# Kernel optimization log

Measured on AMD Instinct MI355X. Metric: run time of the kernel, lower is better.

The kernel has to match this reference:

```python
import jax, jax.numpy as jnp
import numpy as np

EPS = 1e-15
ATANH_CLIP = 1.0 - 1e-5
C = 1.0  # ball.c = |k|, k = -1.0
SQC = 1.0  # sqrt(C)


def _artanh(x):
    return jnp.arctanh(jnp.clip(x, -ATANH_CLIP, ATANH_CLIP))


def _norm(x):
    return jnp.linalg.norm(x, axis=-1, keepdims=True)


def mobius_add(x, y):
    x2 = jnp.sum(x * x, axis=-1, keepdims=True)
    y2 = jnp.sum(y * y, axis=-1, keepdims=True)
    xy = jnp.sum(x * y, axis=-1, keepdims=True)
    num = (1.0 + 2.0 * C * xy + C * y2) * x + (1.0 - C * x2) * y
    den = 1.0 + 2.0 * C * xy + (C ** 2) * x2 * y2
    return num / jnp.maximum(den, EPS)


def mobius_matvec(M, x):
    # x: [..., d_in], M: [d_out, d_in]
    x_norm = jnp.maximum(_norm(x), EPS)
    mx = x @ M.T
    mx_norm_raw = _norm(mx)
    mx_norm = jnp.maximum(mx_norm_raw, EPS)
    res = jnp.tanh(mx_norm / x_norm * _artanh(SQC * x_norm)) * mx / (mx_norm * SQC)
    return jnp.where(mx_norm_raw <= EPS, 0.0, res)


def mobius_pointwise_mul(w, x):
    x_norm = jnp.maximum(_norm(x), EPS)
    wx = w * x
    wx_norm_raw = _norm(wx)
    wx_norm = jnp.maximum(wx_norm_raw, EPS)
    res = jnp.tanh(wx_norm / x_norm * _artanh(SQC * x_norm)) * wx / (wx_norm * SQC)
    return jnp.where(wx_norm_raw <= EPS, 0.0, res)


def expmap0(u):
    un = jnp.maximum(_norm(u), EPS)
    return jnp.tanh(SQC * un) * u / (SQC * un)


def logmap0(y):
    yn = jnp.maximum(_norm(y), EPS)
    return _artanh(SQC * yn) * y / (SQC * yn)


def one_rnn_transform(W, h, U, x, b):
    Wh = mobius_matvec(W, h)
    Ux = mobius_matvec(U, x)
    return mobius_add(mobius_add(Wh, Ux), b)


def gru_cell(x, hx, weight_ih, weight_hh, bias):
    W_ir, W_ih, W_iz = jnp.split(weight_ih, 3, axis=0)
    W_hr, W_hh, W_hz = jnp.split(weight_hh, 3, axis=0)
    b_r, b_h, b_z = bias[0], bias[1], bias[2]
    z_t = jax.nn.sigmoid(logmap0(one_rnn_transform(W_hz, hx, W_iz, x, b_z)))
    r_t = jax.nn.sigmoid(logmap0(one_rnn_transform(W_hr, hx, W_ir, x, b_r)))
    rh_t = mobius_pointwise_mul(r_t, hx)
    h_tilde = one_rnn_transform(W_hh, rh_t, W_ih, x, b_h)
    delta_h = mobius_add(-hx, h_tilde)
    return mobius_add(hx, mobius_pointwise_mul(z_t, delta_h))


def gru_layer(x_seq, h0, weight_ih, weight_hh, bias):
    def step(hx, xt):
        h = gru_cell(xt, hx, weight_ih, weight_hh, bias)
        return h, h
    h_last, outs = jax.lax.scan(step, h0, x_seq)
    return outs, h_last


def setup_inputs() -> dict:
    key = jax.random.key(0)
    ks = jax.random.split(key, 8)
    T, B, D, H = 256, 64, 512, 512
    stdv = 1.0 / np.sqrt(H)
    inp = {
        # hyperbolic_input=True -> points must lie inside the unit ball; scale small
        "input": jax.random.normal(ks[0], (T, B, D), jnp.float32) * 0.01,
        "h0": jnp.zeros((2, B, H), jnp.float32),
        "weight_ih_1": jax.random.uniform(ks[1], (3 * H, D), jnp.float32, -stdv, stdv),
        "weight_ih_2": jax.random.uniform(ks[2], (3 * H, H), jnp.float32, -stdv, stdv),
        "weight_hh_1": jax.random.uniform(ks[3], (3 * H, H), jnp.float32, -stdv, stdv),
        "weight_hh_2": jax.random.uniform(ks[4], (3 * H, H), jnp.float32, -stdv, stdv),
        # biases initialized as expmap0(randn * 1e-5)
        "bias_1": expmap0(jax.random.normal(ks[5], (3, H), jnp.float32) * 1e-5),
        "bias_2": expmap0(jax.random.normal(ks[6], (3, H), jnp.float32) * 1e-5),
    }
    return inp


def reference(input, h0, weight_ih_1, weight_ih_2, weight_hh_1, weight_hh_2, bias_1, bias_2):
    # hyperbolic_input=True and hyperbolic_hidden_state0=True -> no initial expmap0
    out1, h_last1 = gru_layer(input, h0[0], weight_ih_1, weight_hh_1, bias_1)
    out2, h_last2 = gru_layer(out1, h0[1], weight_ih_2, weight_hh_2, bias_2)
    ht = jnp.stack([h_last1, h_last2])
    return out2, ht
```

## Files before the change

kernel.cpp:

```cpp
#include <hip/hip_runtime.h>
#include <hip/hip_fp16.h>
#include <math.h>
#include <stdint.h>


#define T_  256
#define B_  64
#define H_  512
#define G3_ 1536
#define EPSF 1e-15f
#define CLIPF (1.0f - 1e-5f)
#define SCOPE_AGENT __HIP_MEMORY_SCOPE_AGENT

typedef _Float16 v2h __attribute__((ext_vector_type(2)));

__device__ __forceinline__ float fdot2_(unsigned int w, unsigned int h, float c){
#if __has_builtin(__builtin_amdgcn_fdot2)
  return __builtin_amdgcn_fdot2(__builtin_bit_cast(v2h, w), __builtin_bit_cast(v2h, h), c, false);
#else
  const __half2 wh = __builtin_bit_cast(__half2, w);
  const __half2 hh = __builtin_bit_cast(__half2, h);
  return c + __low2float(wh)*__low2float(hh) + __high2float(wh)*__high2float(hh);
#endif
}

__device__ __forceinline__ float artanh_c(float x){
  x = fminf(fmaxf(x, -CLIPF), CLIPF);
  return 0.5f * logf((1.0f + x) / (1.0f - x));
}
__device__ __forceinline__ float sigmoidf_(float x){ return 1.0f/(1.0f+expf(-x)); }
__device__ __forceinline__ float hsum4(float4 v){ return (v.x+v.y)+(v.z+v.w); }

__device__ __forceinline__ void postf(unsigned long long* p, float x, unsigned tag){
  unsigned long long v = ((unsigned long long)tag << 32) |
                         (unsigned long long)__float_as_uint(x);
  __hip_atomic_store(p, v, __ATOMIC_RELAXED, SCOPE_AGENT);
}
__device__ __forceinline__ float pollf(const unsigned long long* p, unsigned tag){
  unsigned long long v = __hip_atomic_load(p, __ATOMIC_RELAXED, SCOPE_AGENT);
  while ((unsigned)(v >> 32) != tag)
    v = __hip_atomic_load(p, __ATOMIC_RELAXED, SCOPE_AGENT);
  return __uint_as_float((unsigned)v);
}

template<int NS>
__device__ __forceinline__ void wave_reduce_store(float (&v)[NS], float* red, int tid){
  #pragma unroll
  for (int off = 32; off > 0; off >>= 1)
    #pragma unroll
    for (int s = 0; s < NS; s++) v[s] += __shfl_xor(v[s], off);
  if ((tid & 63) == 0)
    #pragma unroll
    for (int s = 0; s < NS; s++) red[s*8 + (tid >> 6)] = v[s];
}

__global__ void k_prep_ih(const float* __restrict__ Wih, float* __restrict__ WihT){
  int i = blockIdx.x * blockDim.x + threadIdx.x;
  if (i >= H_ * G3_) return;
  int k = i / G3_, n = i % G3_;
  WihT[i] = Wih[n * H_ + k];
}

__device__ __forceinline__ uint4 pack8h(const float* s){
  __half2 p0 = __halves2half2(__float2half_rn(s[0]), __float2half_rn(s[1]));
  __half2 p1 = __halves2half2(__float2half_rn(s[2]), __float2half_rn(s[3]));
  __half2 p2 = __halves2half2(__float2half_rn(s[4]), __float2half_rn(s[5]));
  __half2 p3 = __halves2half2(__float2half_rn(s[6]), __float2half_rn(s[7]));
  uint4 r;
  r.x = __builtin_bit_cast(unsigned int, p0);
  r.y = __builtin_bit_cast(unsigned int, p1);
  r.z = __builtin_bit_cast(unsigned int, p2);
  r.w = __builtin_bit_cast(unsigned int, p3);
  return r;
}

__global__ void k_prep_hhR(const float* __restrict__ Whh, uint4* __restrict__ WzrR,
                           uint4* __restrict__ WhcR){
  int i = blockIdx.x * blockDim.x + threadIdx.x;
  if (i < 65536){
    int w = i >> 14, rem = i & 16383;
    int ii = rem >> 9, tid = rem & 511;
    int c = tid & 255, ks = tid >> 8;
    int j = 128*w + (c & 127);
    int row = (c < 128) ? (1024 + j) : j;
    int k0 = ks*256 + ii*8;
    WzrR[i] = pack8h(Whh + row*H_ + k0);
  } else {
    int e = i - 65536;
    int w = e >> 13, rem = e & 8191;
    int q = rem >> 11, rem2 = rem & 2047;
    int ii = rem2 >> 7, c = rem2 & 127;
    int row = 512 + 128*w + c;
    int k0 = q*128 + ii*8;
    WhcR[e] = pack8h(Whh + row*H_ + k0);
  }
}

__global__ __launch_bounds__(256) void k_gemm(const float* __restrict__ A,
                                              const float* __restrict__ Bt,
                                              float* __restrict__ C){
  const int N = G3_, K = H_;
  const int mbase = blockIdx.x * 64, nbase = blockIdx.y * 64;
  __shared__ float As[32][65];
  __shared__ float Bs[32][65];
  const int tid = threadIdx.x;
  const int tm = tid >> 4, tn = tid & 15;
  float acc[4][4] = {};
  for (int k0 = 0; k0 < K; k0 += 32){
    #pragma unroll
    for (int i = 0; i < 8; i++){
      int e = tid + 256*i;
      int m = e >> 5, k = e & 31;
      As[k][m] = A[(size_t)(mbase + m) * K + k0 + k];
      int kk = e >> 6, n = e & 63;
      Bs[kk][n] = Bt[(size_t)(k0 + kk) * N + nbase + n];
    }
    __syncthreads();
    #pragma unroll
    for (int kk = 0; kk < 32; kk++){
      float av[4], bv[4];
      #pragma unroll
      for (int i = 0; i < 4; i++) av[i] = As[kk][tm*4+i];
      #pragma unroll
      for (int j = 0; j < 4; j++) bv[j] = Bs[kk][tn*4+j];
      #pragma unroll
      for (int i = 0; i < 4; i++)
        #pragma unroll
        for (int j = 0; j < 4; j++)
          acc[i][j] = fmaf(av[i], bv[j], acc[i][j]);
    }
    __syncthreads();
  }
  #pragma unroll
  for (int i = 0; i < 4; i++)
    #pragma unroll
    for (int j = 0; j < 4; j++)
      C[(size_t)(mbase + tm*4 + i) * N + nbase + tn*4 + j] = acc[i][j];
}

__global__ void k_nonlin(const float* __restrict__ X, float* __restrict__ D){
  const int row = blockIdx.x;
  const int lane = threadIdx.x;
  const float* x = X + (size_t)row * H_;
  float s = 0.0f;
  for (int k = lane; k < H_; k += 64){ float v = x[k]; s = fmaf(v, v, s); }
  #pragma unroll
  for (int off = 32; off > 0; off >>= 1) s += __shfl_xor(s, off);
  const float xn = fmaxf(sqrtf(s), EPSF);
  const float art = artanh_c(xn);
  float* drow = D + (size_t)row * G3_;
  for (int g = 0; g < 3; g++){
    float* mx = drow + g * H_;
    float s2 = 0.0f;
    for (int k = lane; k < H_; k += 64){ float v = mx[k]; s2 = fmaf(v, v, s2); }
    #pragma unroll
    for (int off = 32; off > 0; off >>= 1) s2 += __shfl_xor(s2, off);
    const float raw = sqrtf(s2);
    const float mn = fmaxf(raw, EPSF);
    const float scale = (raw <= EPSF) ? 0.0f : (tanhf(mn / xn * art) / mn);
    for (int k = lane; k < H_; k += 64) mx[k] *= scale;
  }
}

__global__ __launch_bounds__(512, 1) void k_scan(
    const float* __restrict__ D,
    const uint4* __restrict__ WzrR,
    const uint4* __restrict__ WhcR,
    const float* __restrict__ bias,
    const float* __restrict__ h0,
    float* __restrict__ outbuf,
    float* __restrict__ hlast,
    unsigned long long* __restrict__ hS,
    unsigned long long* __restrict__ wvS,
    unsigned long long* __restrict__ S1s,
    unsigned long long* __restrict__ S3s,
    unsigned long long* __restrict__ S4s)
{
  const int blk = blockIdx.x;
  const int b = blk & 63, w = blk >> 6;
  const int tid = threadIdx.x;
  const int lane = tid & 63, wave = tid >> 6;
  __shared__ __align__(16) __half hh[H_];
  __shared__ __align__(16) float hf[H_];
  __shared__ __align__(16) __half wvh[H_];
  __shared__ __align__(16) float ph[512];
  __shared__ __align__(16) float red[96];
  __shared__ __align__(16) float redW[8];
  __shared__ __align__(16) float xr[16];

  unsigned long long* hRow  = hS  + b*512;
  unsigned long long* wvRow = wvS + b*512;
  unsigned long long* s1Row = S1s + b*64;
  unsigned long long* s3Row = S3s + b*64;
  unsigned long long* s4Row = S4s + b*64;

  const int ks = tid >> 8;
  const int c2 = tid & 127, q = tid >> 7;
  const uint4* wAb = WzrR + (size_t)w*32*512 + tid;
  const uint4* wBb = WhcR + ((size_t)(w*4 + q)*16)*128 + c2;
  uint4 wA[32];
  #pragma unroll
  for (int i = 0; i < 32; i++) wA[i] = wAb[i*512];
  uint4 wB[16];
  #pragma unroll
  for (int i = 0; i < 16; i++) wB[i] = wBb[i*128];

  {
    const float hv0 = h0[b*H_ + tid];
    hf[tid] = hv0;
    hh[tid] = __float2half_rn(hv0);
  }
  const int jg = 128*w + (tid & 127);
  const bool isZ = (tid < 128);
  const bool isGate = (tid < 256);
  const float bval = isGate ? (isZ ? bias[1024 + jg] : bias[jg]) : 0.f;
  const float bcj  = isZ ? bias[512 + jg] : 0.f;
  float B2own, BC2;
  {
    const float vz = bias[1024 + tid], vr = bias[tid], vc = bias[512 + tid];
    float vb[3] = { vz*vz, vr*vr, vc*vc };
    wave_reduce_store<3>(vb, red, tid);
    __syncthreads();
    const float4* p = (const float4*)red;
    const float B2z = hsum4(p[0]) + hsum4(p[1]);
    const float B2r = hsum4(p[2]) + hsum4(p[3]);
    BC2 = hsum4(p[4]) + hsum4(p[5]);
    B2own = isZ ? B2z : B2r;
    __syncthreads();
  }

  const uint4* hh4 = (const uint4*)hh;
  const uint4* wv4 = (const uint4*)wvh;
  const float* Dbase = D + (size_t)b * G3_;

  float zreg = 0.f;
  for (int t = 0; t < T_; t++){
    const unsigned tag = (unsigned)(t + 1);
    const float* U = Dbase + (size_t)t * (B_ * G3_);
    const float yg = isGate ? U[(isZ ? 1024 : 0) + jg] : 0.f;
    const float yc = isZ ? U[512 + jg] : 0.f;

    if (t > 0){
      const float hv = pollf(hRow + tid, (unsigned)t);
      hf[tid] = hv;
      hh[tid] = __float2half_rn(hv);
    }
    __syncthreads();
    const float hv = hf[tid];

    float ap = 0.f;
    #pragma unroll
    for (int i = 0; i < 32; i++){
      const uint4 wr = wA[i];
      const uint4 hp = hh4[ks*32 + i];
      ap = fdot2_(wr.x, hp.x, ap);
      ap = fdot2_(wr.y, hp.y, ap);
      ap = fdot2_(wr.z, hp.z, ap);
      ap = fdot2_(wr.w, hp.w, ap);
    }
    ph[tid] = ap;
    __syncthreads();
    const float a = isGate ? (ph[tid] + ph[tid + 256]) : 0.f;

    {
      float v[11];
      v[0] = hv*hv;
      #pragma unroll
      for (int s = 1; s < 11; s++) v[s] = 0.f;
      if (isGate){
        const int o = isZ ? 1 : 6;
        v[o] = a*a; v[o+1] = a*yg; v[o+2] = yg*yg; v[o+3] = a*bval; v[o+4] = yg*bval;
      }
      wave_reduce_store<11>(v, red, tid);
    }
    __syncthreads();
    float H2;
    { const float4* p = (const float4*)red; H2 = hsum4(p[0]) + hsum4(p[1]); }
    if (wave == 0 && lane < 10){
      float s = 0.f;
      const float* r = red + (1 + lane)*8;
      #pragma unroll
      for (int i = 0; i < 8; i++) s += r[i];
      postf(s1Row + w*16 + lane, s, tag);
    }
    if (wave == 0){
      const int wgi = lane >> 4, s = lane & 15;
      float v = (s < 10) ? pollf(s1Row + wgi*16 + s, tag) : 0.f;
      v += __shfl_xor(v, 16);
      v += __shfl_xor(v, 32);
      if (lane < 16) xr[lane] = v;
    }
    __syncthreads();

    const float xn = fmaxf(sqrtf(H2), EPSF);
    const float art_h = artanh_c(xn);
    if (isGate){
      const int o = isZ ? 0 : 5;
      const float A2 = xr[o], AY = xr[o+1], Yy2 = xr[o+2], AB = xr[o+3], YB = xr[o+4];
      const float mraw = sqrtf(A2);
      const float mnc = fmaxf(mraw, EPSF);
      const float alpha = (mraw <= EPSF) ? 0.f : (tanhf(mnc/xn*art_h)/mnc);
      const float X2 = alpha*alpha*A2, XY = alpha*AY, XB = alpha*AB;
      const float cA1 = 1.f + 2.f*XY + Yy2, cB1 = 1.f - X2;
      const float den1 = fmaxf(1.f + 2.f*XY + X2*Yy2, EPSF), id1 = 1.f/den1;
      const float T2 = fmaxf((cA1*cA1*X2 + 2.f*cA1*cB1*XY + cB1*cB1*Yy2)*id1*id1, 0.f);
      const float TB = (cA1*XB + cB1*YB)*id1;
      const float cA2 = 1.f + 2.f*TB + B2own, cB2 = 1.f - T2;
      const float den2 = fmaxf(1.f + 2.f*TB + T2*B2own, EPSF), id2 = 1.f/den2;
      const float U2 = fmaxf((cA2*cA2*T2 + 2.f*cA2*cB2*TB + cB2*cB2*B2own)*id2*id2, 0.f);
      const float un = fmaxf(sqrtf(U2), EPSF);
      const float lsc = artanh_c(un)/un;
      const float t1el = (cA1*(alpha*a) + cB1*yg)*id1;
      const float uel  = (cA2*t1el + cB2*bval)*id2;
      const float g = sigmoidf_(lsc*uel);
      if (isZ) zreg = g;
      else postf(wvRow + jg, g * hf[jg], tag);
    }
    const float wvv = pollf(wvRow + tid, tag);
    wvh[tid] = __float2half_rn(wvv);
    {
      float v1[1] = { wvv*wvv };
      wave_reduce_store<1>(v1, redW, tid);
    }
    __syncthreads();
    float W2;
    { const float4* p = (const float4*)redW; W2 = hsum4(p[0]) + hsum4(p[1]); }
    const float wraw = sqrtf(W2);
    const float wn = fmaxf(wraw, EPSF);
    const float mu = (wraw <= EPSF) ? 0.f : (tanhf(wn/xn*art_h)/wn);
    const float rhn = fmaxf(mu*wraw, EPSF);

    float cp = 0.f;
    #pragma unroll
    for (int i = 0; i < 16; i++){
      const uint4 wr = wB[i];
      const uint4 rp = wv4[q*16 + i];
      cp = fdot2_(wr.x, rp.x, cp);
      cp = fdot2_(wr.y, rp.y, cp);
      cp = fdot2_(wr.z, rp.z, cp);
      cp = fdot2_(wr.w, rp.w, cp);
    }
    ph[tid] = cp;
    __syncthreads();
    float cel = 0.f, hj = 0.f;
    if (isZ){
      cel = mu * (ph[tid] + ph[tid+128] + ph[tid+256] + ph[tid+384]);
      hj  = hf[jg];
    }
    {
      float v[8] = { cel*cel, cel*yc, yc*yc, cel*bcj, yc*bcj, hj*cel, hj*yc, hj*bcj };
      wave_reduce_store<8>(v, red, tid);
    }
    __syncthreads();
    if (wave == 0 && lane < 8){
      float s = 0.f;
      const float* r = red + lane*8;
      #pragma unroll
      for (int i = 0; i < 8; i++) s += r[i];
      postf(s3Row + w*16 + lane, s, tag);
    }
    if (wave == 0){
      const int wgi = lane >> 4, s = lane & 15;
      float v = (s < 8) ? pollf(s3Row + wgi*16 + s, tag) : 0.f;
      v += __shfl_xor(v, 16);
      v += __shfl_xor(v, 32);
      if (lane < 16) xr[lane] = v;
    }
    __syncthreads();
    const float C2 = xr[0], CY = xr[1], Y2c = xr[2], CB = xr[3],
                YBc = xr[4], HC = xr[5], HYd = xr[6], HBd = xr[7];
    const float craw = sqrtf(C2);
    const float cmn2 = fmaxf(craw, EPSF);
    const float alc = (craw <= EPSF) ? 0.f : (tanhf(cmn2/rhn*artanh_c(rhn))/cmn2);
    const float X2c = alc*alc*C2, XYc = alc*CY, XBc = alc*CB, HXc = alc*HC;
    const float cA1c = 1.f + 2.f*XYc + Y2c, cB1c = 1.f - X2c;
    const float den1c = fmaxf(1.f + 2.f*XYc + X2c*Y2c, EPSF), id1c = 1.f/den1c;
    const float T2c = fmaxf((cA1c*cA1c*X2c + 2.f*cA1c*cB1c*XYc + cB1c*cB1c*Y2c)*id1c*id1c, 0.f);
    const float TBc = (cA1c*XBc + cB1c*YBc)*id1c;
    const float HT1 = (cA1c*HXc + cB1c*HYd)*id1c;
    const float cA2c = 1.f + 2.f*TBc + BC2, cB2c = 1.f - T2c;
    const float den2c = fmaxf(1.f + 2.f*TBc + T2c*BC2, EPSF), id2c = 1.f/den2c;
    const float HTL2 = fmaxf((cA2c*cA2c*T2c + 2.f*cA2c*cB2c*TBc + cB2c*cB2c*BC2)*id2c*id2c, 0.f);
    const float HHTL = (cA2c*HT1 + cB2c*HBd)*id2c;
    const float cAd = 1.f - 2.f*HHTL + HTL2, cBd = 1.f - H2;
    const float dend = fmaxf(1.f - 2.f*HHTL + H2*HTL2, EPSF), idd = 1.f/dend;
    float del = 0.f, w2el = 0.f;
    if (isZ){
      const float t1cel = (cA1c*(alc*cel) + cB1c*yc)*id1c;
      const float htlel = (cA2c*t1cel + cB2c*bcj)*id2c;
      del = (cAd*(-hj) + cBd*htlel)*idd;
      w2el = zreg*del;
    }
    {
      float v[3] = { del*del, w2el*w2el, hj*w2el };
      wave_reduce_store<3>(v, red, tid);
    }
    __syncthreads();
    if (wave == 0 && lane < 3){
      float s = 0.f;
      const float* r = red + lane*8;
      #pragma unroll
      for (int i = 0; i < 8; i++) s += r[i];
      postf(s4Row + w*16 + lane, s, tag);
    }
    if (wave == 0){
      const int wgi = lane >> 4, s = lane & 15;
      float v = (s < 3) ? pollf(s4Row + wgi*16 + s, tag) : 0.f;
      v += __shfl_xor(v, 16);
      v += __shfl_xor(v, 32);
      if (lane < 16) xr[lane] = v;
    }
    __syncthreads();
    const float D2v = xr[0], W22 = xr[1], HW = xr[2];
    const float dnv = fmaxf(sqrtf(D2v), EPSF);
    const float w2raw = sqrtf(W22);
    const float w2n = fmaxf(w2raw, EPSF);
    const float nu = (w2raw <= EPSF) ? 0.f : (tanhf(w2n/dnv*artanh_c(dnv))/w2n);
    const float Y2f = nu*nu*W22, XYf = nu*HW;
    const float cAf = 1.f + 2.f*XYf + Y2f, cBf = 1.f - H2;
    const float denf = fmaxf(1.f + 2.f*XYf + H2*Y2f, EPSF), idf = 1.f/denf;
    if (isZ){
      const float hnew = (cAf*hj + cBf*(nu*w2el))*idf;
      outbuf[(size_t)(t*B_ + b)*H_ + jg] = hnew;
      postf(hRow + jg, hnew, tag);
      if (t == T_-1) hlast[b*H_ + jg] = hnew;
    }
  }
}

extern "C" void kernel_launch(void* const* d_in, const int* in_sizes, int n_in,
                              void* d_out, int out_size, void* d_ws, size_t ws_size,
                              hipStream_t stream){
  (void)in_sizes; (void)n_in; (void)out_size; (void)ws_size;
  const float* input = (const float*)d_in[0];
  const float* h0    = (const float*)d_in[1];
  const float* wih1  = (const float*)d_in[2];
  const float* wih2  = (const float*)d_in[3];
  const float* whh1  = (const float*)d_in[4];
  const float* whh2  = (const float*)d_in[5];
  const float* bias1 = (const float*)d_in[6];
  const float* bias2 = (const float*)d_in[7];
  float* out = (float*)d_out;

  float* A_    = (float*)d_ws;
  float* Dbuf  = A_ + 786432;
  uint4* WzrR  = (uint4*)(Dbuf + 25165824);
  uint4* WhcR  = WzrR + 65536;
  float* comm0 = (float*)(WhcR + 32768);
  unsigned long long* hS1  = (unsigned long long*)comm0;
  unsigned long long* wvS1 = hS1  + 32768;
  unsigned long long* S1a  = wvS1 + 32768;
  unsigned long long* S3a  = S1a  + 4096;
  unsigned long long* S4a  = S3a  + 4096;
  unsigned long long* hS2  = S4a  + 4096;
  unsigned long long* wvS2 = hS2  + 32768;
  unsigned long long* S1b  = wvS2 + 32768;
  unsigned long long* S3b  = S1b  + 4096;
  unsigned long long* S4b  = S3b  + 4096;

  float* out1 = out;
  float* ht   = out + (size_t)T_ * B_ * H_;

  k_prep_ih<<<3072, 256, 0, stream>>>(wih1, A_);
  k_gemm<<<dim3(256, 24), 256, 0, stream>>>(input, A_, Dbuf);
  k_nonlin<<<T_*B_, 64, 0, stream>>>(input, Dbuf);
  k_prep_hhR<<<384, 256, 0, stream>>>(whh1, WzrR, WhcR);
  k_scan<<<256, 512, 0, stream>>>(Dbuf, WzrR, WhcR, bias1, h0, out1, ht,
                                  hS1, wvS1, S1a, S3a, S4a);

  k_prep_ih<<<3072, 256, 0, stream>>>(wih2, A_);
  k_gemm<<<dim3(256, 24), 256, 0, stream>>>(out1, A_, Dbuf);
  k_nonlin<<<T_*B_, 64, 0, stream>>>(out1, Dbuf);
  k_prep_hhR<<<384, 256, 0, stream>>>(whh2, WzrR, WhcR);
  k_scan<<<256, 512, 0, stream>>>(Dbuf, WzrR, WhcR, bias2, h0 + B_*H_, out, ht + B_*H_,
                                  hS2, wvS2, S1b, S3b, S4b);
}
```

Baseline: 7.784 ms.

## Replicate full hidden state per block and exchange pre-activation vectors instead of partial sums

Each of the four blocks that share a batch row now holds the whole 512-wide hidden state and computes all gate, reduction and update math redundantly, so it no longer needs to gather h, the r*h vector, or scalar partial sums across blocks. Cross-block traffic is cut to three vector exchanges per step: the z and r matvec outputs and the candidate matvec output, with each block reading its own slice from shared memory. This removes several global-memory handshake rounds on the serial timestep chain, at the cost of duplicated elementwise work and wider polling of 512-element vectors. Tags are offset per layer so the communication buffers can be reused by the second layer.

```diff
diff --git a/kernel.cpp b/kernel.cpp
--- a/kernel.cpp
+++ b/kernel.cpp
@@ -30,6 +30,10 @@
 }
 __device__ __forceinline__ float sigmoidf_(float x){ return 1.0f/(1.0f+expf(-x)); }
 __device__ __forceinline__ float hsum4(float4 v){ return (v.x+v.y)+(v.z+v.w); }
+__device__ __forceinline__ float sum8(const float* r){
+  const float4* p = (const float4*)r;
+  return hsum4(p[0]) + hsum4(p[1]);
+}
 
 __device__ __forceinline__ void postf(unsigned long long* p, float x, unsigned tag){
   unsigned long long v = ((unsigned long long)tag << 32) |
@@ -52,6 +56,27 @@
   if ((tid & 63) == 0)
     #pragma unroll
     for (int s = 0; s < NS; s++) red[s*8 + (tid >> 6)] = v[s];
+}
+
+__device__ __forceinline__ float gate_val(float a, float y, float bv,
+    float A2, float AY, float Y2, float AB, float YB, float B2,
+    float xn, float art_h){
+  const float mraw = sqrtf(A2);
+  const float mnc = fmaxf(mraw, EPSF);
+  const float alpha = (mraw <= EPSF) ? 0.f : (tanhf(mnc/xn*art_h)/mnc);
+  const float X2 = alpha*alpha*A2, XY = alpha*AY, XB = alpha*AB;
+  const float cA1 = 1.f + 2.f*XY + Y2, cB1 = 1.f - X2;
+  const float den1 = fmaxf(1.f + 2.f*XY + X2*Y2, EPSF), id1 = 1.f/den1;
+  const float T2 = fmaxf((cA1*cA1*X2 + 2.f*cA1*cB1*XY + cB1*cB1*Y2)*id1*id1, 0.f);
+  const float TB = (cA1*XB + cB1*YB)*id1;
+  const float cA2 = 1.f + 2.f*TB + B2, cB2 = 1.f - T2;
+  const float den2 = fmaxf(1.f + 2.f*TB + T2*B2, EPSF), id2 = 1.f/den2;
+  const float U2 = fmaxf((cA2*cA2*T2 + 2.f*cA2*cB2*TB + cB2*cB2*B2)*id2*id2, 0.f);
+  const float un = fmaxf(sqrtf(U2), EPSF);
+  const float lsc = artanh_c(un)/un;
+  const float t1el = (cA1*(alpha*a) + cB1*y)*id1;
+  const float uel  = (cA2*t1el + cB2*bv)*id2;
+  return sigmoidf_(lsc*uel);
 }
 
 __global__ void k_prep_ih(const float* __restrict__ Wih, float* __restrict__ WihT){
@@ -170,29 +195,26 @@
     const float* __restrict__ h0,
     float* __restrict__ outbuf,
     float* __restrict__ hlast,
-    unsigned long long* __restrict__ hS,
-    unsigned long long* __restrict__ wvS,
-    unsigned long long* __restrict__ S1s,
-    unsigned long long* __restrict__ S3s,
-    unsigned long long* __restrict__ S4s)
+    unsigned long long* __restrict__ AZ,
+    unsigned long long* __restrict__ AR,
+    unsigned long long* __restrict__ CEL,
+    unsigned tagbase)
 {
   const int blk = blockIdx.x;
   const int b = blk & 63, w = blk >> 6;
   const int tid = threadIdx.x;
-  const int lane = tid & 63, wave = tid >> 6;
   __shared__ __align__(16) __half hh[H_];
-  __shared__ __align__(16) float hf[H_];
   __shared__ __align__(16) __half wvh[H_];
   __shared__ __align__(16) float ph[512];
-  __shared__ __align__(16) float red[96];
+  __shared__ __align__(16) float redE[72];
+  __shared__ __align__(16) float redA[48];
   __shared__ __align__(16) float redW[8];
-  __shared__ __align__(16) float xr[16];
-
-  unsigned long long* hRow  = hS  + b*512;
-  unsigned long long* wvRow = wvS + b*512;
-  unsigned long long* s1Row = S1s + b*64;
-  unsigned long long* s3Row = S3s + b*64;
-  unsigned long long* s4Row = S4s + b*64;
+  __shared__ __align__(16) float redC[32];
+  __shared__ __align__(16) float redD[24];
+
+  unsigned long long* azRow = AZ  + (size_t)b*512;
+  unsigned long long* arRow = AR  + (size_t)b*512;
+  unsigned long long* ceRow = CEL + (size_t)b*512;
 
   const int ks = tid >> 8;
   const int c2 = tid & 127, q = tid >> 7;
@@ -205,48 +227,28 @@
   #pragma unroll
   for (int i = 0; i < 16; i++) wB[i] = wBb[i*128];
 
+  float h_own = h0[b*H_ + tid];
+  hh[tid] = __float2half_rn(h_own);
+
+  const float bz = bias[1024 + tid], br = bias[tid], bc = bias[512 + tid];
   {
-    const float hv0 = h0[b*H_ + tid];
-    hf[tid] = hv0;
-    hh[tid] = __float2half_rn(hv0);
+    float vb[3] = { bz*bz, br*br, bc*bc };
+    wave_reduce_store<3>(vb, redD, tid);
   }
-  const int jg = 128*w + (tid & 127);
-  const bool isZ = (tid < 128);
-  const bool isGate = (tid < 256);
-  const float bval = isGate ? (isZ ? bias[1024 + jg] : bias[jg]) : 0.f;
-  const float bcj  = isZ ? bias[512 + jg] : 0.f;
-  float B2own, BC2;
-  {
-    const float vz = bias[1024 + tid], vr = bias[tid], vc = bias[512 + tid];
-    float vb[3] = { vz*vz, vr*vr, vc*vc };
-    wave_reduce_store<3>(vb, red, tid);
-    __syncthreads();
-    const float4* p = (const float4*)red;
-    const float B2z = hsum4(p[0]) + hsum4(p[1]);
-    const float B2r = hsum4(p[2]) + hsum4(p[3]);
-    BC2 = hsum4(p[4]) + hsum4(p[5]);
-    B2own = isZ ? B2z : B2r;
-    __syncthreads();
-  }
+  __syncthreads();
+  const float B2z = sum8(redD), B2r = sum8(redD+8), BC2 = sum8(redD+16);
+  __syncthreads();
 
   const uint4* hh4 = (const uint4*)hh;
   const uint4* wv4 = (const uint4*)wvh;
   const float* Dbase = D + (size_t)b * G3_;
-
-  float zreg = 0.f;
+  const int jA = 128*w + (tid & 127);
+  const bool own = ((tid >> 7) == w);
+
   for (int t = 0; t < T_; t++){
-    const unsigned tag = (unsigned)(t + 1);
+    const unsigned tag = tagbase + (unsigned)t + 1u;
     const float* U = Dbase + (size_t)t * (B_ * G3_);
-    const float yg = isGate ? U[(isZ ? 1024 : 0) + jg] : 0.f;
-    const float yc = isZ ? U[512 + jg] : 0.f;
-
-    if (t > 0){
-      const float hv = pollf(hRow + tid, (unsigned)t);
-      hf[tid] = hv;
-      hh[tid] = __float2half_rn(hv);
-    }
-    __syncthreads();
-    const float hv = hf[tid];
+    const float yr = U[tid], yc = U[512 + tid], yz = U[1024 + tid];
 
     float ap = 0.f;
     #pragma unroll
@@ -259,72 +261,58 @@
       ap = fdot2_(wr.w, hp.w, ap);
     }
     ph[tid] = ap;
-    __syncthreads();
-    const float a = isGate ? (ph[tid] + ph[tid + 256]) : 0.f;
-
     {
-      float v[11];
-      v[0] = hv*hv;
-      #pragma unroll
-      for (int s = 1; s < 11; s++) v[s] = 0.f;
-      if (isGate){
-        const int o = isZ ? 1 : 6;
-        v[o] = a*a; v[o+1] = a*yg; v[o+2] = yg*yg; v[o+3] = a*bval; v[o+4] = yg*bval;
-      }
-      wave_reduce_store<11>(v, red, tid);
-    }
-    __syncthreads();
-    float H2;
-    { const float4* p = (const float4*)red; H2 = hsum4(p[0]) + hsum4(p[1]); }
-    if (wave == 0 && lane < 10){
-      float s = 0.f;
-      const float* r = red + (1 + lane)*8;
-      #pragma unroll
-      for (int i = 0; i < 8; i++) s += r[i];
-      postf(s1Row + w*16 + lane, s, tag);
-    }
-    if (wave == 0){
-      const int wgi = lane >> 4, s = lane & 15;
-      float v = (s < 10) ? pollf(s1Row + wgi*16 + s, tag) : 0.f;
-      v += __shfl_xor(v, 16);
-      v += __shfl_xor(v, 32);
-      if (lane < 16) xr[lane] = v;
-    }
-    __syncthreads();
+      float v[9] = { h_own*h_own, yz*yz, yz*bz, yr*yr, yr*br,
+                     yc*yc, yc*bc, h_own*yc, h_own*bc };
+      wave_reduce_store<9>(v, redE, tid);
+    }
+    __syncthreads();
+    if (tid < 256){
+      const float a = ph[tid] + ph[tid + 256];
+      postf(((tid < 128) ? azRow : arRow) + jA, a, tag);
+    }
+    float az, ar;
+    if (own){
+      const int x = tid & 127;
+      az = ph[x]       + ph[x + 256];
+      ar = ph[x + 128] + ph[x + 384];
+    } else {
+      const unsigned long long* pz = azRow + tid;
+      const unsigned long long* pr = arRow + tid;
+      unsigned long long uz = __hip_atomic_load(pz, __ATOMIC_RELAXED, SCOPE_AGENT);
+      unsigned long long ur = __hip_atomic_load(pr, __ATOMIC_RELAXED, SCOPE_AGENT);
+      while ((unsigned)(uz >> 32) != tag)
+        uz = __hip_atomic_load(pz, __ATOMIC_RELAXED, SCOPE_AGENT);
+      while ((unsigned)(ur >> 32) != tag)
+        ur = __hip_atomic_load(pr, __ATOMIC_RELAXED, SCOPE_AGENT);
+      az = __uint_as_float((unsigned)uz);
+      ar = __uint_as_float((unsigned)ur);
+    }
+    {
+      float v[6] = { az*az, az*yz, az*bz, ar*ar, ar*yr, ar*br };
+      wave_reduce_store<6>(v, redA, tid);
+    }
+    __syncthreads();
+    const float H2  = sum8(redE);
+    const float Y2z = sum8(redE+8),  YBz = sum8(redE+16);
+    const float Y2r = sum8(redE+24), YBr = sum8(redE+32);
+    const float Y2c = sum8(redE+40), YBc = sum8(redE+48);
+    const float HYd = sum8(redE+56), HBd = sum8(redE+64);
+    const float A2z = sum8(redA), AYz = sum8(redA+8), ABz = sum8(redA+16);
+    const float A2r = sum8(redA+24), AYr = sum8(redA+32), ABr = sum8(redA+40);
 
     const float xn = fmaxf(sqrtf(H2), EPSF);
     const float art_h = artanh_c(xn);
-    if (isGate){
-      const int o = isZ ? 0 : 5;
-      const float A2 = xr[o], AY = xr[o+1], Yy2 = xr[o+2], AB = xr[o+3], YB = xr[o+4];
-      const float mraw = sqrtf(A2);
-      const float mnc = fmaxf(mraw, EPSF);
-      const float alpha = (mraw <= EPSF) ? 0.f : (tanhf(mnc/xn*art_h)/mnc);
-      const float X2 = alpha*alpha*A2, XY = alpha*AY, XB = alpha*AB;
-      const float cA1 = 1.f + 2.f*XY + Yy2, cB1 = 1.f - X2;
-      const float den1 = fmaxf(1.f + 2.f*XY + X2*Yy2, EPSF), id1 = 1.f/den1;
-      const float T2 = fmaxf((cA1*cA1*X2 + 2.f*cA1*cB1*XY + cB1*cB1*Yy2)*id1*id1, 0.f);
-      const float TB = (cA1*XB + cB1*YB)*id1;
-      const float cA2 = 1.f + 2.f*TB + B2own, cB2 = 1.f - T2;
-      const float den2 = fmaxf(1.f + 2.f*TB + T2*B2own, EPSF), id2 = 1.f/den2;
-      const float U2 = fmaxf((cA2*cA2*T2 + 2.f*cA2*cB2*TB + cB2*cB2*B2own)*id2*id2, 0.f);
-      const float un = fmaxf(sqrtf(U2), EPSF);
-      const float lsc = artanh_c(un)/un;
-      const float t1el = (cA1*(alpha*a) + cB1*yg)*id1;
-      const float uel  = (cA2*t1el + cB2*bval)*id2;
-      const float g = sigmoidf_(lsc*uel);
-      if (isZ) zreg = g;
-      else postf(wvRow + jg, g * hf[jg], tag);
-    }
-    const float wvv = pollf(wvRow + tid, tag);
+    const float zj = gate_val(az, yz, bz, A2z, AYz, Y2z, ABz, YBz, B2z, xn, art_h);
+    const float rj = gate_val(ar, yr, br, A2r, AYr, Y2r, ABr, YBr, B2r, xn, art_h);
+    const float wvv = rj * h_own;
     wvh[tid] = __float2half_rn(wvv);
     {
       float v1[1] = { wvv*wvv };
       wave_reduce_store<1>(v1, redW, tid);
     }
     __syncthreads();
-    float W2;
-    { const float4* p = (const float4*)redW; W2 = hsum4(p[0]) + hsum4(p[1]); }
+    const float W2 = sum8(redW);
     const float wraw = sqrtf(W2);
     const float wn = fmaxf(wraw, EPSF);
     const float mu = (wraw <= EPSF) ? 0.f : (tanhf(wn/xn*art_h)/wn);
@@ -342,33 +330,24 @@
     }
     ph[tid] = cp;
     __syncthreads();
-    float cel = 0.f, hj = 0.f;
-    if (isZ){
-      cel = mu * (ph[tid] + ph[tid+128] + ph[tid+256] + ph[tid+384]);
-      hj  = hf[jg];
+    if (tid < 128){
+      const float celo = mu * (ph[tid] + ph[tid+128] + ph[tid+256] + ph[tid+384]);
+      postf(ceRow + jA, celo, tag);
+    }
+    float cel;
+    if (own){
+      const int x = tid & 127;
+      cel = mu * (ph[x] + ph[x+128] + ph[x+256] + ph[x+384]);
+    } else {
+      cel = pollf(ceRow + tid, tag);
     }
     {
-      float v[8] = { cel*cel, cel*yc, yc*yc, cel*bcj, yc*bcj, hj*cel, hj*yc, hj*bcj };
-      wave_reduce_store<8>(v, red, tid);
-    }
-    __syncthreads();
-    if (wave == 0 && lane < 8){
-      float s = 0.f;
-      const float* r = red + lane*8;
-      #pragma unroll
-      for (int i = 0; i < 8; i++) s += r[i];
-      postf(s3Row + w*16 + lane, s, tag);
-    }
-    if (wave == 0){
-      const int wgi = lane >> 4, s = lane & 15;
-      float v = (s < 8) ? pollf(s3Row + wgi*16 + s, tag) : 0.f;
-      v += __shfl_xor(v, 16);
-      v += __shfl_xor(v, 32);
-      if (lane < 16) xr[lane] = v;
-    }
-    __syncthreads();
-    const float C2 = xr[0], CY = xr[1], Y2c = xr[2], CB = xr[3],
-                YBc = xr[4], HC = xr[5], HYd = xr[6], HBd = xr[7];
+      float v[4] = { cel*cel, cel*yc, cel*bc, h_own*cel };
+      wave_reduce_store<4>(v, redC, tid);
+    }
+    __syncthreads();
+    const float C2 = sum8(redC), CY = sum8(redC+8),
+                CB = sum8(redC+16), HC = sum8(redC+24);
     const float craw = sqrtf(C2);
     const float cmn2 = fmaxf(craw, EPSF);
     const float alc = (craw <= EPSF) ? 0.f : (tanhf(cmn2/rhn*artanh_c(rhn))/cmn2);
@@ -384,34 +363,16 @@
     const float HHTL = (cA2c*HT1 + cB2c*HBd)*id2c;
     const float cAd = 1.f - 2.f*HHTL + HTL2, cBd = 1.f - H2;
     const float dend = fmaxf(1.f - 2.f*HHTL + H2*HTL2, EPSF), idd = 1.f/dend;
-    float del = 0.f, w2el = 0.f;
-    if (isZ){
-      const float t1cel = (cA1c*(alc*cel) + cB1c*yc)*id1c;
-      const float htlel = (cA2c*t1cel + cB2c*bcj)*id2c;
-      del = (cAd*(-hj) + cBd*htlel)*idd;
-      w2el = zreg*del;
-    }
+    const float t1cel = (cA1c*(alc*cel) + cB1c*yc)*id1c;
+    const float htlel = (cA2c*t1cel + cB2c*bc)*id2c;
+    const float del = (cAd*(-h_own) + cBd*htlel)*idd;
+    const float w2el = zj*del;
     {
-      float v[3] = { del*del, w2el*w2el, hj*w2el };
-      wave_reduce_store<3>(v, red, tid);
-    }
-    __syncthreads();
-    if (wave == 0 && lane < 3){
-      float s = 0.f;
-      const float* r = red + lane*8;
-      #pragma unroll
-      for (int i = 0; i < 8; i++) s += r[i];
-      postf(s4Row + w*16 + lane, s, tag);
-    }
-    if (wave == 0){
-      const int wgi = lane >> 4, s = lane & 15;
-      float v = (s < 3) ? pollf(s4Row + wgi*16 + s, tag) : 0.f;
-      v += __shfl_xor(v, 16);
-      v += __shfl_xor(v, 32);
-      if (lane < 16) xr[lane] = v;
-    }
-    __syncthreads();
-    const float D2v = xr[0], W22 = xr[1], HW = xr[2];
+      float v[3] = { del*del, w2el*w2el, h_own*w2el };
+      wave_reduce_store<3>(v, redD, tid);
+    }
+    __syncthreads();
+    const float D2v = sum8(redD), W22 = sum8(redD+8), HW = sum8(redD+16);
     const float dnv = fmaxf(sqrtf(D2v), EPSF);
     const float w2raw = sqrtf(W22);
     const float w2n = fmaxf(w2raw, EPSF);
@@ -419,12 +380,14 @@
     const float Y2f = nu*nu*W22, XYf = nu*HW;
     const float cAf = 1.f + 2.f*XYf + Y2f, cBf = 1.f - H2;
     const float denf = fmaxf(1.f + 2.f*XYf + H2*Y2f, EPSF), idf = 1.f/denf;
-    if (isZ){
-      const float hnew = (cAf*hj + cBf*(nu*w2el))*idf;
-      outbuf[(size_t)(t*B_ + b)*H_ + jg] = hnew;
-      postf(hRow + jg, hnew, tag);
-      if (t == T_-1) hlast[b*H_ + jg] = hnew;
-    }
+    const float hnew = (cAf*h_own + cBf*(nu*w2el))*idf;
+    h_own = hnew;
+    hh[tid] = __float2half_rn(hnew);
+    if (w == 0){
+      outbuf[(size_t)(t*B_ + b)*H_ + tid] = hnew;
+      if (t == T_-1) hlast[b*H_ + tid] = hnew;
+    }
+    __syncthreads();
   }
 }
 
@@ -446,17 +409,9 @@
   float* Dbuf  = A_ + 786432;
   uint4* WzrR  = (uint4*)(Dbuf + 25165824);
   uint4* WhcR  = WzrR + 65536;
-  float* comm0 = (float*)(WhcR + 32768);
-  unsigned long long* hS1  = (unsigned long long*)comm0;
-  unsigned long long* wvS1 = hS1  + 32768;
-  unsigned long long* S1a  = wvS1 + 32768;
-  unsigned long long* S3a  = S1a  + 4096;
-  unsigned long long* S4a  = S3a  + 4096;
-  unsigned long long* hS2  = S4a  + 4096;
-  unsigned long long* wvS2 = hS2  + 32768;
-  unsigned long long* S1b  = wvS2 + 32768;
-  unsigned long long* S3b  = S1b  + 4096;
-  unsigned long long* S4b  = S3b  + 4096;
+  unsigned long long* AZ  = (unsigned long long*)(WhcR + 32768);
+  unsigned long long* AR  = AZ + 32768;
+  unsigned long long* CEL = AR + 32768;
 
   float* out1 = out;
   float* ht   = out + (size_t)T_ * B_ * H_;
@@ -466,12 +421,12 @@
   k_nonlin<<<T_*B_, 64, 0, stream>>>(input, Dbuf);
   k_prep_hhR<<<384, 256, 0, stream>>>(whh1, WzrR, WhcR);
   k_scan<<<256, 512, 0, stream>>>(Dbuf, WzrR, WhcR, bias1, h0, out1, ht,
-                                  hS1, wvS1, S1a, S3a, S4a);
+                                  AZ, AR, CEL, 0u);
 
   k_prep_ih<<<3072, 256, 0, stream>>>(wih2, A_);
   k_gemm<<<dim3(256, 24), 256, 0, stream>>>(out1, A_, Dbuf);
   k_nonlin<<<T_*B_, 64, 0, stream>>>(out1, Dbuf);
   k_prep_hhR<<<384, 256, 0, stream>>>(whh2, WzrR, WhcR);
   k_scan<<<256, 512, 0, stream>>>(Dbuf, WzrR, WhcR, bias2, h0 + B_*H_, out, ht + B_*H_,
-                                  hS2, wvS2, S1b, S3b, S4b);
-}
+                                  AZ, AR, CEL, 256u);
+}
```

After: 10.89 ms. 1.4x slower.

## Eliminate final cross-block reduction by expanding norms algebraically from precomputed moments

Applied to the files above, without the earlier changes.

The update vector del is a linear combination of hj, cel, yc and bcj with block-uniform coefficients. The kernel therefore precomputes all pairwise (z-weighted) inner products in the earlier cross-workgroup reduction and derives the norms of del and z*del, and their dot with h, in closed form. This removes one global post/poll barrier round and two __syncthreads per timestep of the sequential scan. In exchange the earlier reduction grows from 8 to 22 values, and the quadratic expansion can lose float precision through cancellation.

```diff
diff --git a/kernel.cpp b/kernel.cpp
--- a/kernel.cpp
+++ b/kernel.cpp
@@ -173,8 +173,7 @@
     unsigned long long* __restrict__ hS,
     unsigned long long* __restrict__ wvS,
     unsigned long long* __restrict__ S1s,
-    unsigned long long* __restrict__ S3s,
-    unsigned long long* __restrict__ S4s)
+    unsigned long long* __restrict__ S3s)
 {
   const int blk = blockIdx.x;
   const int b = blk & 63, w = blk >> 6;
@@ -184,15 +183,14 @@
   __shared__ __align__(16) float hf[H_];
   __shared__ __align__(16) __half wvh[H_];
   __shared__ __align__(16) float ph[512];
-  __shared__ __align__(16) float red[96];
+  __shared__ __align__(16) float red[176];
   __shared__ __align__(16) float redW[8];
-  __shared__ __align__(16) float xr[16];
+  __shared__ __align__(16) float xr[32];
 
   unsigned long long* hRow  = hS  + b*512;
   unsigned long long* wvRow = wvS + b*512;
   unsigned long long* s1Row = S1s + b*64;
-  unsigned long long* s3Row = S3s + b*64;
-  unsigned long long* s4Row = S4s + b*64;
+  unsigned long long* s3Row = S3s + b*128;
 
   const int ks = tid >> 8;
   const int c2 = tid & 127, q = tid >> 7;
@@ -348,27 +346,45 @@
       hj  = hf[jg];
     }
     {
-      float v[8] = { cel*cel, cel*yc, yc*yc, cel*bcj, yc*bcj, hj*cel, hj*yc, hj*bcj };
-      wave_reduce_store<8>(v, red, tid);
-    }
-    __syncthreads();
-    if (wave == 0 && lane < 8){
+      const float z2 = zreg*zreg;
+      float v[22] = {
+        cel*cel, cel*yc, yc*yc, cel*bcj, yc*bcj, hj*cel, hj*yc, hj*bcj,
+        z2*hj*hj, z2*hj*cel, z2*hj*yc, z2*hj*bcj,
+        z2*cel*cel, z2*cel*yc, z2*cel*bcj,
+        z2*yc*yc, z2*yc*bcj, z2*bcj*bcj,
+        zreg*hj*hj, zreg*hj*cel, zreg*hj*yc, zreg*hj*bcj };
+      wave_reduce_store<22>(v, red, tid);
+    }
+    __syncthreads();
+    if (wave == 0 && lane < 22){
       float s = 0.f;
       const float* r = red + lane*8;
       #pragma unroll
       for (int i = 0; i < 8; i++) s += r[i];
-      postf(s3Row + w*16 + lane, s, tag);
+      postf(s3Row + w*32 + lane, s, tag);
     }
     if (wave == 0){
       const int wgi = lane >> 4, s = lane & 15;
-      float v = (s < 8) ? pollf(s3Row + wgi*16 + s, tag) : 0.f;
+      float v = (s < 16) ? pollf(s3Row + wgi*32 + s, tag) : 0.f;
       v += __shfl_xor(v, 16);
       v += __shfl_xor(v, 32);
       if (lane < 16) xr[lane] = v;
     }
+    if (wave == 1){
+      const int wgi = lane >> 4, s = 16 + (lane & 15);
+      float v = (s < 22) ? pollf(s3Row + wgi*32 + s, tag) : 0.f;
+      v += __shfl_xor(v, 16);
+      v += __shfl_xor(v, 32);
+      if (lane < 16) xr[16 + lane] = v;
+    }
     __syncthreads();
     const float C2 = xr[0], CY = xr[1], Y2c = xr[2], CB = xr[3],
                 YBc = xr[4], HC = xr[5], HYd = xr[6], HBd = xr[7];
+    const float Z2HH = xr[8],  Z2HC = xr[9],  Z2HY = xr[10], Z2HB = xr[11];
+    const float Z2CC = xr[12], Z2CY = xr[13], Z2CB = xr[14];
+    const float Z2YY = xr[15], Z2YB = xr[16], Z2BB = xr[17];
+    const float ZHH  = xr[18], ZHC  = xr[19], ZHY  = xr[20], ZHB  = xr[21];
+
     const float craw = sqrtf(C2);
     const float cmn2 = fmaxf(craw, EPSF);
     const float alc = (craw <= EPSF) ? 0.f : (tanhf(cmn2/rhn*artanh_c(rhn))/cmn2);
@@ -384,34 +400,20 @@
     const float HHTL = (cA2c*HT1 + cB2c*HBd)*id2c;
     const float cAd = 1.f - 2.f*HHTL + HTL2, cBd = 1.f - H2;
     const float dend = fmaxf(1.f - 2.f*HHTL + H2*HTL2, EPSF), idd = 1.f/dend;
-    float del = 0.f, w2el = 0.f;
-    if (isZ){
-      const float t1cel = (cA1c*(alc*cel) + cB1c*yc)*id1c;
-      const float htlel = (cA2c*t1cel + cB2c*bcj)*id2c;
-      del = (cAd*(-hj) + cBd*htlel)*idd;
-      w2el = zreg*del;
-    }
-    {
-      float v[3] = { del*del, w2el*w2el, hj*w2el };
-      wave_reduce_store<3>(v, red, tid);
-    }
-    __syncthreads();
-    if (wave == 0 && lane < 3){
-      float s = 0.f;
-      const float* r = red + lane*8;
-      #pragma unroll
-      for (int i = 0; i < 8; i++) s += r[i];
-      postf(s4Row + w*16 + lane, s, tag);
-    }
-    if (wave == 0){
-      const int wgi = lane >> 4, s = lane & 15;
-      float v = (s < 3) ? pollf(s4Row + wgi*16 + s, tag) : 0.f;
-      v += __shfl_xor(v, 16);
-      v += __shfl_xor(v, 32);
-      if (lane < 16) xr[lane] = v;
-    }
-    __syncthreads();
-    const float D2v = xr[0], W22 = xr[1], HW = xr[2];
+
+    const float Pc = id2c*cA2c*id1c*cA1c*alc;
+    const float Qc = id2c*cA2c*id1c*cB1c;
+    const float Rc = id2c*cB2c;
+    const float Af = -idd*cAd;
+    const float Bf = idd*cBd*Pc, Cf = idd*cBd*Qc, Ef = idd*cBd*Rc;
+    const float D2v = fmaxf(
+        Af*Af*H2 + Bf*Bf*C2 + Cf*Cf*Y2c + Ef*Ef*BC2
+      + 2.f*(Af*Bf*HC + Af*Cf*HYd + Af*Ef*HBd + Bf*Cf*CY + Bf*Ef*CB + Cf*Ef*YBc), 0.f);
+    const float W22 = fmaxf(
+        Af*Af*Z2HH + Bf*Bf*Z2CC + Cf*Cf*Z2YY + Ef*Ef*Z2BB
+      + 2.f*(Af*Bf*Z2HC + Af*Cf*Z2HY + Af*Ef*Z2HB + Bf*Cf*Z2CY + Bf*Ef*Z2CB + Cf*Ef*Z2YB), 0.f);
+    const float HW = Af*ZHH + Bf*ZHC + Cf*ZHY + Ef*ZHB;
+
     const float dnv = fmaxf(sqrtf(D2v), EPSF);
     const float w2raw = sqrtf(W22);
     const float w2n = fmaxf(w2raw, EPSF);
@@ -420,6 +422,10 @@
     const float cAf = 1.f + 2.f*XYf + Y2f, cBf = 1.f - H2;
     const float denf = fmaxf(1.f + 2.f*XYf + H2*Y2f, EPSF), idf = 1.f/denf;
     if (isZ){
+      const float t1cel = (cA1c*(alc*cel) + cB1c*yc)*id1c;
+      const float htlel = (cA2c*t1cel + cB2c*bcj)*id2c;
+      const float del = (cAd*(-hj) + cBd*htlel)*idd;
+      const float w2el = zreg*del;
       const float hnew = (cAf*hj + cBf*(nu*w2el))*idf;
       outbuf[(size_t)(t*B_ + b)*H_ + jg] = hnew;
       postf(hRow + jg, hnew, tag);
@@ -451,12 +457,10 @@
   unsigned long long* wvS1 = hS1  + 32768;
   unsigned long long* S1a  = wvS1 + 32768;
   unsigned long long* S3a  = S1a  + 4096;
-  unsigned long long* S4a  = S3a  + 4096;
-  unsigned long long* hS2  = S4a  + 4096;
+  unsigned long long* hS2  = S3a  + 8192;
   unsigned long long* wvS2 = hS2  + 32768;
   unsigned long long* S1b  = wvS2 + 32768;
   unsigned long long* S3b  = S1b  + 4096;
-  unsigned long long* S4b  = S3b  + 4096;
 
   float* out1 = out;
   float* ht   = out + (size_t)T_ * B_ * H_;
@@ -466,12 +470,12 @@
   k_nonlin<<<T_*B_, 64, 0, stream>>>(input, Dbuf);
   k_prep_hhR<<<384, 256, 0, stream>>>(whh1, WzrR, WhcR);
   k_scan<<<256, 512, 0, stream>>>(Dbuf, WzrR, WhcR, bias1, h0, out1, ht,
-                                  hS1, wvS1, S1a, S3a, S4a);
+                                  hS1, wvS1, S1a, S3a);
 
   k_prep_ih<<<3072, 256, 0, stream>>>(wih2, A_);
   k_gemm<<<dim3(256, 24), 256, 0, stream>>>(out1, A_, Dbuf);
   k_nonlin<<<T_*B_, 64, 0, stream>>>(out1, Dbuf);
   k_prep_hhR<<<384, 256, 0, stream>>>(whh2, WzrR, WhcR);
   k_scan<<<256, 512, 0, stream>>>(Dbuf, WzrR, WhcR, bias2, h0 + B_*H_, out, ht + B_*H_,
-                                  hS2, wvS2, S1b, S3b, S4b);
-}
+                                  hS2, wvS2, S1b, S3b);
+}
```

Result: slower. 8.707 ms (+11.9%).
